# Optimization experiments

Hardware: AMD Instinct MI355X
Metric: run time of the kernel (lower is better)

## Reference

```python
import jax, jax.numpy as jnp
import numpy as np

B, C, W, H = 16, 512, 32, 32


def spatial_shift1(y):
    # y: [B, W, H, C]; quartile-wise shifts with edge rows/cols left unchanged
    c = y.shape[-1]
    cq = c // 4
    p0 = jnp.concatenate([y[:, :1, :, 0*cq:1*cq], y[:, :-1, :, 0*cq:1*cq]], axis=1)  # w <- w-1
    p1 = jnp.concatenate([y[:, 1:, :, 1*cq:2*cq], y[:, -1:, :, 1*cq:2*cq]], axis=1)  # w <- w+1
    p2 = jnp.concatenate([y[:, :, :1, 2*cq:3*cq], y[:, :, :-1, 2*cq:3*cq]], axis=2)  # h <- h-1
    p3 = jnp.concatenate([y[:, :, 1:, 3*cq:], y[:, :, -1:, 3*cq:]], axis=2)          # h <- h+1
    return jnp.concatenate([p0, p1, p2, p3], axis=-1)


def spatial_shift2(y):
    # same as shift1 with w/h roles swapped
    c = y.shape[-1]
    cq = c // 4
    p0 = jnp.concatenate([y[:, :, :1, 0*cq:1*cq], y[:, :, :-1, 0*cq:1*cq]], axis=2)  # h <- h-1
    p1 = jnp.concatenate([y[:, :, 1:, 1*cq:2*cq], y[:, :, -1:, 1*cq:2*cq]], axis=2)  # h <- h+1
    p2 = jnp.concatenate([y[:, :1, :, 2*cq:3*cq], y[:, :-1, :, 2*cq:3*cq]], axis=1)  # w <- w-1
    p3 = jnp.concatenate([y[:, 1:, :, 3*cq:], y[:, -1:, :, 3*cq:]], axis=1)          # w <- w+1
    return jnp.concatenate([p0, p1, p2, p3], axis=-1)


def setup_inputs() -> dict:
    key = jax.random.key(0)
    ks = jax.random.split(key, 9)
    s = 0.02
    return {
        "x": jax.random.normal(ks[0], (B, C, W, H), dtype=jnp.float32),
        "w1": jax.random.normal(ks[1], (3 * C, C), dtype=jnp.float32) * s,
        "b1": jax.random.normal(ks[2], (3 * C,), dtype=jnp.float32) * s,
        "wa": jax.random.normal(ks[3], (C, C), dtype=jnp.float32) * s,
        "ba": jax.random.normal(ks[4], (C,), dtype=jnp.float32) * s,
        "wb": jax.random.normal(ks[5], (3 * C, C), dtype=jnp.float32) * s,
        "bb": jax.random.normal(ks[6], (3 * C,), dtype=jnp.float32) * s,
        "w2": jax.random.normal(ks[7], (C, C), dtype=jnp.float32) * s,
        "b2": jax.random.normal(ks[8], (C,), dtype=jnp.float32) * s,
    }


def reference(x, w1, b1, wa, ba, wb, bb, w2, b2):
    c = x.shape[1]
    xp = jnp.transpose(x, (0, 2, 3, 1))                     # [B, W, H, C]
    y = jnp.einsum("bwhc,oc->bwho", xp, w1) + b1            # [B, W, H, 3C]
    x1 = spatial_shift1(y[..., :c])
    x2 = spatial_shift2(y[..., c:2 * c])
    x3 = y[..., 2 * c:]
    # SplitAttention: descriptor a = sum over branches and spatial positions
    a = jnp.sum(x1 + x2 + x3, axis=(1, 2))                  # [B, C]
    hat = jax.nn.gelu(a @ wa.T + ba, approximate=False) @ wb.T + bb  # [B, 3C]
    bar = jax.nn.softmax(hat.reshape(-1, 3, c), axis=1)     # softmax over k=3
    g = bar[:, :, None, None, :]                            # [B, 3, 1, 1, C]
    out = g[:, 0] * x1 + g[:, 1] * x2 + g[:, 2] * x3        # [B, W, H, C]
    z = jnp.einsum("bwhc,oc->bwho", out, w2) + b2           # [B, W, H, C]
    return jnp.transpose(z, (0, 3, 1, 2))                   # [B, C, W, H]
```

## Files before the change

kernel.cpp:

```cpp
#include <hip/hip_runtime.h>
#include <stdint.h>

typedef __bf16 bf16x8 __attribute__((ext_vector_type(8)));
typedef float f32x4 __attribute__((ext_vector_type(4)));

#define B_ 16
#define C_ 512
#define S_ 1024
#define N1 1536

__device__ inline unsigned short f2b(float f) {
    unsigned int u = __builtin_bit_cast(unsigned int, f);
    unsigned int lsb = (u >> 16) & 1u;
    u += 0x7fffu + lsb;
    return (unsigned short)(u >> 16);
}
__device__ inline float b2f(unsigned int s) {
    unsigned int u = (s & 0xffffu) << 16;
    return __builtin_bit_cast(float, u);
}

__global__ void transpose_convert_x(const float* __restrict__ x, unsigned short* __restrict__ xT) {
    __shared__ float tile[32][33];
    int b = blockIdx.z;
    int c0 = blockIdx.y * 32;
    int s0 = blockIdx.x * 32;
    int tx = threadIdx.x, ty = threadIdx.y;
    const float* xp = x + ((size_t)b * C_ + c0) * S_ + s0;
#pragma unroll
    for (int i = 0; i < 4; i++)
        tile[ty + i * 8][tx] = xp[(size_t)(ty + i * 8) * S_ + tx];
    __syncthreads();
    unsigned short* op = xT + ((size_t)b * S_ + s0) * C_ + c0;
#pragma unroll
    for (int i = 0; i < 4; i++)
        op[(size_t)(ty + i * 8) * C_ + tx] = f2b(tile[tx][ty + i * 8]);
}

__global__ void convert_f32_bf16(const float* __restrict__ src, unsigned short* __restrict__ dst, int n4) {
    int i = blockIdx.x * blockDim.x + threadIdx.x;
    if (i < n4) {
        float4 v = ((const float4*)src)[i];
        ((ushort4*)dst)[i] = make_ushort4(f2b(v.x), f2b(v.y), f2b(v.z), f2b(v.w));
    }
}

__global__ void zero_f32(float* __restrict__ p, int n) {
    int i = blockIdx.x * blockDim.x + threadIdx.x;
    if (i < n) p[i] = 0.0f;
}

template <bool TRANS_OUT>
__global__ __launch_bounds__(256) void gemm_bf16(
    const unsigned short* __restrict__ A,
    const unsigned short* __restrict__ Wt,
    const float* __restrict__ bias,
    void* __restrict__ Cout,
    int N)
{
    const int K = 512;
    __shared__ __align__(16) unsigned short As[128 * 40];
    __shared__ __align__(16) unsigned short Bs[128 * 40];
    int m0 = blockIdx.x * 128;
    int n0 = blockIdx.y * 128;
    int tid = threadIdx.x;
    int lane = tid & 63, wid = tid >> 6;
    int wm = (wid >> 1) * 64, wn = (wid & 1) * 64;
    int quad = lane >> 4, l16 = lane & 15;

    f32x4 acc[4][4] = {};

    for (int kt = 0; kt < K; kt += 32) {
        __syncthreads();
#pragma unroll
        for (int r = 0; r < 2; r++) {
            int ch = tid + r * 256;
            int m = ch >> 2, kc = ch & 3;
            *(uint4*)(&As[m * 40 + kc * 8]) = *(const uint4*)(&A[(size_t)(m0 + m) * K + kt + kc * 8]);
            *(uint4*)(&Bs[m * 40 + kc * 8]) = *(const uint4*)(&Wt[(size_t)(n0 + m) * K + kt + kc * 8]);
        }
        __syncthreads();
        bf16x8 af[4], bf[4];
#pragma unroll
        for (int t = 0; t < 4; t++) {
            af[t] = *(const bf16x8*)(&As[(wm + t * 16 + l16) * 40 + quad * 8]);
            bf[t] = *(const bf16x8*)(&Bs[(wn + t * 16 + l16) * 40 + quad * 8]);
        }
#pragma unroll
        for (int mt = 0; mt < 4; mt++)
#pragma unroll
            for (int nt = 0; nt < 4; nt++)
                acc[mt][nt] = __builtin_amdgcn_mfma_f32_16x16x32_bf16(af[mt], bf[nt], acc[mt][nt], 0, 0, 0);
    }

#pragma unroll
    for (int mt = 0; mt < 4; mt++) {
#pragma unroll
        for (int nt = 0; nt < 4; nt++) {
            int n = n0 + wn + nt * 16 + l16;
            float bv = bias[n];
            int mbase = m0 + wm + mt * 16 + quad * 4;
            if (!TRANS_OUT) {
                unsigned short* Y = (unsigned short*)Cout;
#pragma unroll
                for (int r = 0; r < 4; r++)
                    Y[(size_t)(mbase + r) * N + n] = f2b(acc[mt][nt][r] + bv);
            } else {
                float* Z = (float*)Cout;
                int b = mbase >> 10;
                int s = mbase & 1023;
                float4 v = make_float4(acc[mt][nt][0] + bv, acc[mt][nt][1] + bv,
                                       acc[mt][nt][2] + bv, acc[mt][nt][3] + bv);
                *(float4*)(&Z[((size_t)(b * 512 + n)) * 1024 + s]) = v;
            }
        }
    }
}


__global__ void asum_kernel(const unsigned short* __restrict__ y, float* __restrict__ a) {
    int b = blockIdx.y;
    int w0 = blockIdx.x * 2;
    int t = threadIdx.x;
    int c = t * 2;
    int q = c >> 7;
    int dw1 = (q == 0) ? -1 : (q == 1) ? 1 : 0;
    int dh1 = (q == 2) ? -1 : (q == 3) ? 1 : 0;
    int dh2 = (q == 0) ? -1 : (q == 1) ? 1 : 0;
    int dw2 = (q == 2) ? -1 : (q == 3) ? 1 : 0;
    float s0 = 0.f, s1 = 0.f;
    size_t base = (size_t)b * S_;
    for (int p = 0; p < 64; p++) {
        int w = w0 + (p >> 5);
        int h = p & 31;
        int w1i = min(max(w + dw1, 0), 31), h1i = min(max(h + dh1, 0), 31);
        int w2i = min(max(w + dw2, 0), 31), h2i = min(max(h + dh2, 0), 31);
        unsigned int v1 = *(const unsigned int*)&y[(base + w1i * 32 + h1i) * N1 + c];
        unsigned int v2 = *(const unsigned int*)&y[(base + w2i * 32 + h2i) * N1 + 512 + c];
        unsigned int v3 = *(const unsigned int*)&y[(base + w * 32 + h) * N1 + 1024 + c];
        s0 += b2f(v1) + b2f(v2) + b2f(v3);
        s1 += b2f(v1 >> 16) + b2f(v2 >> 16) + b2f(v3 >> 16);
    }
    atomicAdd(&a[b * 512 + c], s0);
    atomicAdd(&a[b * 512 + c + 1], s1);
}

__global__ __launch_bounds__(256) void mlp_layer1(
    const float* __restrict__ a, const float* __restrict__ wa,
    const float* __restrict__ ba, float* __restrict__ h)
{
    int gw = (blockIdx.x * 256 + threadIdx.x) >> 6;
    int lane = threadIdx.x & 63;
    int b = gw >> 9;
    int o = gw & 511;
    const float4* wr = (const float4*)(wa + (size_t)o * 512);
    const float4* ar = (const float4*)(a + (size_t)b * 512);
    float4 w0 = wr[lane * 2], w1 = wr[lane * 2 + 1];
    float4 a0 = ar[lane * 2], a1 = ar[lane * 2 + 1];
    float dot = w0.x * a0.x + w0.y * a0.y + w0.z * a0.z + w0.w * a0.w
              + w1.x * a1.x + w1.y * a1.y + w1.z * a1.z + w1.w * a1.w;
#pragma unroll
    for (int off = 32; off; off >>= 1) dot += __shfl_down(dot, off);
    if (lane == 0) {
        float v = dot + ba[o];
        h[(size_t)b * 512 + o] = 0.5f * v * (1.0f + erff(v * 0.7071067811865475f));
    }
}

__global__ __launch_bounds__(256) void mlp_layer2(
    const float* __restrict__ h, const float* __restrict__ wb,
    const float* __restrict__ bb, float* __restrict__ hat)
{
    int gw = (blockIdx.x * 256 + threadIdx.x) >> 6;
    int lane = threadIdx.x & 63;
    int b = gw / 1536;
    int o = gw - b * 1536;
    const float4* wr = (const float4*)(wb + (size_t)o * 512);
    const float4* hr = (const float4*)(h + (size_t)b * 512);
    float4 w0 = wr[lane * 2], w1 = wr[lane * 2 + 1];
    float4 h0 = hr[lane * 2], h1 = hr[lane * 2 + 1];
    float dot = w0.x * h0.x + w0.y * h0.y + w0.z * h0.z + w0.w * h0.w
              + w1.x * h1.x + w1.y * h1.y + w1.z * h1.z + w1.w * h1.w;
#pragma unroll
    for (int off = 32; off; off >>= 1) dot += __shfl_down(dot, off);
    if (lane == 0)
        hat[(size_t)b * 1536 + o] = dot + bb[o];
}

__global__ __launch_bounds__(256) void softmax_gate(
    const float* __restrict__ hat, float* __restrict__ g)
{
    int i = blockIdx.x * 256 + threadIdx.x;
    int b = i >> 9, c = i & 511;
    float h0 = hat[(size_t)b * 1536 + c];
    float h1 = hat[(size_t)b * 1536 + 512 + c];
    float h2 = hat[(size_t)b * 1536 + 1024 + c];
    float mx = fmaxf(h0, fmaxf(h1, h2));
    float e0 = __expf(h0 - mx), e1 = __expf(h1 - mx), e2 = __expf(h2 - mx);
    float inv = 1.0f / (e0 + e1 + e2);
    g[(b * 3 + 0) * 512 + c] = e0 * inv;
    g[(b * 3 + 1) * 512 + c] = e1 * inv;
    g[(b * 3 + 2) * 512 + c] = e2 * inv;
}

__global__ void combine_kernel(const unsigned short* __restrict__ y,
                               const float* __restrict__ g,
                               unsigned short* __restrict__ outT)
{
    int b = blockIdx.y;
    int w = blockIdx.x;
    int t = threadIdx.x;
    int c = t * 2;
    int q = c >> 7;
    int dw1 = (q == 0) ? -1 : (q == 1) ? 1 : 0;
    int dh1 = (q == 2) ? -1 : (q == 3) ? 1 : 0;
    int dh2 = (q == 0) ? -1 : (q == 1) ? 1 : 0;
    int dw2 = (q == 2) ? -1 : (q == 3) ? 1 : 0;
    float g00 = g[(b * 3 + 0) * 512 + c], g01 = g[(b * 3 + 0) * 512 + c + 1];
    float g10 = g[(b * 3 + 1) * 512 + c], g11 = g[(b * 3 + 1) * 512 + c + 1];
    float g20 = g[(b * 3 + 2) * 512 + c], g21 = g[(b * 3 + 2) * 512 + c + 1];
    int w1i = min(max(w + dw1, 0), 31);
    int w2i = min(max(w + dw2, 0), 31);
    size_t base = (size_t)b * S_;
    for (int h = 0; h < 32; h++) {
        int h1i = min(max(h + dh1, 0), 31);
        int h2i = min(max(h + dh2, 0), 31);
        unsigned int v1 = *(const unsigned int*)&y[(base + w1i * 32 + h1i) * N1 + c];
        unsigned int v2 = *(const unsigned int*)&y[(base + w2i * 32 + h2i) * N1 + 512 + c];
        unsigned int v3 = *(const unsigned int*)&y[(base + w * 32 + h) * N1 + 1024 + c];
        float o0 = g00 * b2f(v1) + g10 * b2f(v2) + g20 * b2f(v3);
        float o1 = g01 * b2f(v1 >> 16) + g11 * b2f(v2 >> 16) + g21 * b2f(v3 >> 16);
        unsigned int ov = (unsigned int)f2b(o0) | ((unsigned int)f2b(o1) << 16);
        *(unsigned int*)&outT[(base + w * 32 + h) * 512 + c] = ov;
    }
}

extern "C" void kernel_launch(void* const* d_in, const int* in_sizes, int n_in,
                              void* d_out, int out_size, void* d_ws, size_t ws_size,
                              hipStream_t stream) {
    const float* x  = (const float*)d_in[0];
    const float* w1 = (const float*)d_in[1];
    const float* b1 = (const float*)d_in[2];
    const float* wa = (const float*)d_in[3];
    const float* ba = (const float*)d_in[4];
    const float* wb = (const float*)d_in[5];
    const float* bb = (const float*)d_in[6];
    const float* w2 = (const float*)d_in[7];
    const float* b2 = (const float*)d_in[8];
    float* out = (float*)d_out;

    char* ws = (char*)d_ws;
    unsigned short* xT   = (unsigned short*)(ws);
    unsigned short* w1b  = (unsigned short*)(ws + 16777216);
    unsigned short* w2b  = (unsigned short*)(ws + 18350080);
    unsigned short* y    = (unsigned short*)(ws + 18874368);
    float* a_buf         = (float*)(ws + 69206016);
    float* g_buf         = (float*)(ws + 69238784);
    float* h_buf         = (float*)(ws + 69337088);
    float* hat_buf       = (float*)(ws + 69369856);
    unsigned short* outT = (unsigned short*)(ws + 69468160);

    transpose_convert_x<<<dim3(32, 16, 16), dim3(32, 8), 0, stream>>>(x, xT);
    convert_f32_bf16<<<dim3(768), dim3(256), 0, stream>>>(w1, w1b, 196608);
    convert_f32_bf16<<<dim3(256), dim3(256), 0, stream>>>(w2, w2b, 65536);
    gemm_bf16<false><<<dim3(128, 12), dim3(256), 0, stream>>>(xT, w1b, b1, (void*)y, 1536);
    zero_f32<<<dim3(32), dim3(256), 0, stream>>>(a_buf, 8192);
    asum_kernel<<<dim3(16, 16), dim3(256), 0, stream>>>(y, a_buf);
    mlp_layer1<<<dim3(2048), dim3(256), 0, stream>>>(a_buf, wa, ba, h_buf);
    mlp_layer2<<<dim3(6144), dim3(256), 0, stream>>>(h_buf, wb, bb, hat_buf);
    softmax_gate<<<dim3(32), dim3(256), 0, stream>>>(hat_buf, g_buf);
    combine_kernel<<<dim3(32, 16), dim3(256), 0, stream>>>(y, g_buf, outT);
    gemm_bf16<true><<<dim3(128, 4), dim3(256), 0, stream>>>(outT, w2b, b2, (void*)out, 512);
}
```

Before: 217.5 us.

## Fuse shifted-sum descriptor into GEMM epilogue, use direct-to-LDS loads, merge small kernels

```diff
diff --git a/kernel.cpp b/kernel.cpp
--- a/kernel.cpp
+++ b/kernel.cpp
@@ -18,6 +18,13 @@
 __device__ inline float b2f(unsigned int s) {
     unsigned int u = (s & 0xffffu) << 16;
     return __builtin_bit_cast(float, u);
+}
+
+__device__ inline void gl_lds16(const unsigned short* g, unsigned short* l) {
+    __builtin_amdgcn_global_load_lds(
+        (const __attribute__((address_space(1))) void*)(g),
+        (__attribute__((address_space(3))) void*)(l),
+        16, 0, 0);
 }
 
 __global__ void transpose_convert_x(const float* __restrict__ x, unsigned short* __restrict__ xT) {
@@ -37,60 +44,71 @@
         op[(size_t)(ty + i * 8) * C_ + tx] = f2b(tile[tx][ty + i * 8]);
 }
 
-__global__ void convert_f32_bf16(const float* __restrict__ src, unsigned short* __restrict__ dst, int n4) {
-    int i = blockIdx.x * blockDim.x + threadIdx.x;
-    if (i < n4) {
-        float4 v = ((const float4*)src)[i];
-        ((ushort4*)dst)[i] = make_ushort4(f2b(v.x), f2b(v.y), f2b(v.z), f2b(v.w));
-    }
-}
-
-__global__ void zero_f32(float* __restrict__ p, int n) {
-    int i = blockIdx.x * blockDim.x + threadIdx.x;
-    if (i < n) p[i] = 0.0f;
-}
-
-template <bool TRANS_OUT>
+__global__ __launch_bounds__(256) void misc_prep(
+    const float* __restrict__ w1, const float* __restrict__ w2,
+    unsigned short* __restrict__ w1b, unsigned short* __restrict__ w2b,
+    float* __restrict__ sums)
+{
+    int i = blockIdx.x * 256 + threadIdx.x;
+    if (i < 196608) {
+        float4 v = ((const float4*)w1)[i];
+        ((ushort4*)w1b)[i] = make_ushort4(f2b(v.x), f2b(v.y), f2b(v.z), f2b(v.w));
+    } else if (i < 262144) {
+        int j = i - 196608;
+        float4 v = ((const float4*)w2)[j];
+        ((ushort4*)w2b)[j] = make_ushort4(f2b(v.x), f2b(v.y), f2b(v.z), f2b(v.w));
+    } else if (i < 292864) {
+        int j = i - 262144;
+        ((float4*)sums)[j] = make_float4(0.f, 0.f, 0.f, 0.f);
+    }
+}
+
+template <bool TRANS_OUT, bool DO_SUMS>
 __global__ __launch_bounds__(256) void gemm_bf16(
     const unsigned short* __restrict__ A,
     const unsigned short* __restrict__ Wt,
     const float* __restrict__ bias,
-    void* __restrict__ Cout,
-    int N)
+    void* __restrict__ Cout, int N,
+    float* __restrict__ Tsum, float* __restrict__ H0, float* __restrict__ H31,
+    float* __restrict__ C0, float* __restrict__ C31)
 {
     const int K = 512;
-    __shared__ __align__(16) unsigned short As[128 * 40];
-    __shared__ __align__(16) unsigned short Bs[128 * 40];
+    __shared__ __align__(16) unsigned short As[128 * 32];
+    __shared__ __align__(16) unsigned short Bs[128 * 32];
     int m0 = blockIdx.x * 128;
     int n0 = blockIdx.y * 128;
     int tid = threadIdx.x;
     int lane = tid & 63, wid = tid >> 6;
     int wm = (wid >> 1) * 64, wn = (wid & 1) * 64;
     int quad = lane >> 4, l16 = lane & 15;
+    int ch0 = wid * 128 + lane;
+    const unsigned short* Ab = A + (size_t)m0 * K;
+    const unsigned short* Bb = Wt + (size_t)n0 * K;
 
     f32x4 acc[4][4] = {};
 
     for (int kt = 0; kt < K; kt += 32) {
         __syncthreads();
 #pragma unroll
-        for (int r = 0; r < 2; r++) {
-            int ch = tid + r * 256;
+        for (int i = 0; i < 2; i++) {
+            int ch = ch0 + i * 64;
             int m = ch >> 2, kc = ch & 3;
-            *(uint4*)(&As[m * 40 + kc * 8]) = *(const uint4*)(&A[(size_t)(m0 + m) * K + kt + kc * 8]);
-            *(uint4*)(&Bs[m * 40 + kc * 8]) = *(const uint4*)(&Wt[(size_t)(n0 + m) * K + kt + kc * 8]);
+            size_t go = (size_t)m * K + kt + kc * 8;
+            gl_lds16(Ab + go, &As[ch * 8]);
+            gl_lds16(Bb + go, &Bs[ch * 8]);
         }
         __syncthreads();
-        bf16x8 af[4], bf[4];
+        bf16x8 af[4], bfr[4];
 #pragma unroll
         for (int t = 0; t < 4; t++) {
-            af[t] = *(const bf16x8*)(&As[(wm + t * 16 + l16) * 40 + quad * 8]);
-            bf[t] = *(const bf16x8*)(&Bs[(wn + t * 16 + l16) * 40 + quad * 8]);
+            af[t]  = *(const bf16x8*)&As[(wm + t * 16 + l16) * 32 + quad * 8];
+            bfr[t] = *(const bf16x8*)&Bs[(wn + t * 16 + l16) * 32 + quad * 8];
         }
 #pragma unroll
         for (int mt = 0; mt < 4; mt++)
 #pragma unroll
             for (int nt = 0; nt < 4; nt++)
-                acc[mt][nt] = __builtin_amdgcn_mfma_f32_16x16x32_bf16(af[mt], bf[nt], acc[mt][nt], 0, 0, 0);
+                acc[mt][nt] = __builtin_amdgcn_mfma_f32_16x16x32_bf16(af[mt], bfr[nt], acc[mt][nt], 0, 0, 0);
     }
 
 #pragma unroll
@@ -115,55 +133,92 @@
             }
         }
     }
-}
-
-
-__global__ void asum_kernel(const unsigned short* __restrict__ y, float* __restrict__ a) {
-    int b = blockIdx.y;
-    int w0 = blockIdx.x * 2;
+
+    if (DO_SUMS) {
+        int b = m0 >> 10;
+        int wlo = (m0 & 1023) >> 5;
+#pragma unroll
+        for (int nt = 0; nt < 4; nt++) {
+            int n = n0 + wn + nt * 16 + l16;
+            float bv = bias[n];
+            float tT = 0.f;
+#pragma unroll
+            for (int mt = 0; mt < 4; mt++)
+#pragma unroll
+                for (int r = 0; r < 4; r++) tT += acc[mt][nt][r] + bv;
+            tT += __shfl_xor(tT, 16);
+            tT += __shfl_xor(tT, 32);
+            if (quad == 0) {
+                atomicAdd(&Tsum[b * 1536 + n], tT);
+                float th0 = acc[0][nt][0] + acc[2][nt][0] + 2.f * bv;
+                atomicAdd(&H0[b * 1536 + n], th0);
+            }
+            if (quad == 3) {
+                float th31 = acc[1][nt][3] + acc[3][nt][3] + 2.f * bv;
+                atomicAdd(&H31[b * 1536 + n], th31);
+            }
+            if (wlo == 0 && wm == 0) {
+                float tc = 0.f;
+#pragma unroll
+                for (int mt = 0; mt < 2; mt++)
+#pragma unroll
+                    for (int r = 0; r < 4; r++) tc += acc[mt][nt][r] + bv;
+                tc += __shfl_xor(tc, 16);
+                tc += __shfl_xor(tc, 32);
+                if (quad == 0) atomicAdd(&C0[b * 1536 + n], tc);
+            }
+            if (wlo == 28 && wm == 64) {
+                float tc = 0.f;
+#pragma unroll
+                for (int mt = 2; mt < 4; mt++)
+#pragma unroll
+                    for (int r = 0; r < 4; r++) tc += acc[mt][nt][r] + bv;
+                tc += __shfl_xor(tc, 16);
+                tc += __shfl_xor(tc, 32);
+                if (quad == 0) atomicAdd(&C31[b * 1536 + n], tc);
+            }
+        }
+    }
+}
+
+__global__ __launch_bounds__(256) void mlp_layer1(
+    const float* __restrict__ sums, const float* __restrict__ wa,
+    const float* __restrict__ ba, float* __restrict__ h)
+{
+    __shared__ float sa[512];
+    int b = blockIdx.x >> 7;
     int t = threadIdx.x;
-    int c = t * 2;
-    int q = c >> 7;
-    int dw1 = (q == 0) ? -1 : (q == 1) ? 1 : 0;
-    int dh1 = (q == 2) ? -1 : (q == 3) ? 1 : 0;
-    int dh2 = (q == 0) ? -1 : (q == 1) ? 1 : 0;
-    int dw2 = (q == 2) ? -1 : (q == 3) ? 1 : 0;
-    float s0 = 0.f, s1 = 0.f;
-    size_t base = (size_t)b * S_;
-    for (int p = 0; p < 64; p++) {
-        int w = w0 + (p >> 5);
-        int h = p & 31;
-        int w1i = min(max(w + dw1, 0), 31), h1i = min(max(h + dh1, 0), 31);
-        int w2i = min(max(w + dw2, 0), 31), h2i = min(max(h + dh2, 0), 31);
-        unsigned int v1 = *(const unsigned int*)&y[(base + w1i * 32 + h1i) * N1 + c];
-        unsigned int v2 = *(const unsigned int*)&y[(base + w2i * 32 + h2i) * N1 + 512 + c];
-        unsigned int v3 = *(const unsigned int*)&y[(base + w * 32 + h) * N1 + 1024 + c];
-        s0 += b2f(v1) + b2f(v2) + b2f(v3);
-        s1 += b2f(v1 >> 16) + b2f(v2 >> 16) + b2f(v3 >> 16);
-    }
-    atomicAdd(&a[b * 512 + c], s0);
-    atomicAdd(&a[b * 512 + c + 1], s1);
-}
-
-__global__ __launch_bounds__(256) void mlp_layer1(
-    const float* __restrict__ a, const float* __restrict__ wa,
-    const float* __restrict__ ba, float* __restrict__ h)
-{
-    int gw = (blockIdx.x * 256 + threadIdx.x) >> 6;
-    int lane = threadIdx.x & 63;
-    int b = gw >> 9;
-    int o = gw & 511;
+    const float* Tp   = sums;
+    const float* H0p  = sums + 24576;
+    const float* H31p = sums + 49152;
+    const float* C0p  = sums + 73728;
+    const float* C31p = sums + 98304;
+#pragma unroll
+    for (int j = 0; j < 2; j++) {
+        int c = t + j * 256;
+        int q = c >> 7;
+        int n1 = b * 1536 + c;
+        float t123 = Tp[n1] + Tp[n1 + 512] + Tp[n1 + 1024];
+        float sC1 = C0p[n1] - C31p[n1];
+        float sH1 = H0p[n1] - H31p[n1];
+        float sC2 = C0p[n1 + 512] - C31p[n1 + 512];
+        float sH2 = H0p[n1 + 512] - H31p[n1 + 512];
+        float e = (q < 2) ? (sC1 + sH2) : (sH1 + sC2);
+        sa[c] = t123 + ((q & 1) ? -e : e);
+    }
+    __syncthreads();
+    int lane = t & 63, wid = t >> 6;
+    int o = (blockIdx.x & 127) * 4 + wid;
     const float4* wr = (const float4*)(wa + (size_t)o * 512);
-    const float4* ar = (const float4*)(a + (size_t)b * 512);
-    float4 w0 = wr[lane * 2], w1 = wr[lane * 2 + 1];
-    float4 a0 = ar[lane * 2], a1 = ar[lane * 2 + 1];
+    float4 w0 = wr[lane * 2], w1v = wr[lane * 2 + 1];
+    float4 a0 = ((const float4*)sa)[lane * 2], a1 = ((const float4*)sa)[lane * 2 + 1];
     float dot = w0.x * a0.x + w0.y * a0.y + w0.z * a0.z + w0.w * a0.w
-              + w1.x * a1.x + w1.y * a1.y + w1.z * a1.z + w1.w * a1.w;
+              + w1v.x * a1.x + w1v.y * a1.y + w1v.z * a1.z + w1v.w * a1.w;
 #pragma unroll
     for (int off = 32; off; off >>= 1) dot += __shfl_down(dot, off);
     if (lane == 0) {
         float v = dot + ba[o];
-        h[(size_t)b * 512 + o] = 0.5f * v * (1.0f + erff(v * 0.7071067811865475f));
+        h[b * 512 + o] = 0.5f * v * (1.0f + erff(v * 0.7071067811865475f));
     }
 }
 
@@ -187,51 +242,52 @@
         hat[(size_t)b * 1536 + o] = dot + bb[o];
 }
 
-__global__ __launch_bounds__(256) void softmax_gate(
-    const float* __restrict__ hat, float* __restrict__ g)
-{
-    int i = blockIdx.x * 256 + threadIdx.x;
-    int b = i >> 9, c = i & 511;
-    float h0 = hat[(size_t)b * 1536 + c];
-    float h1 = hat[(size_t)b * 1536 + 512 + c];
-    float h2 = hat[(size_t)b * 1536 + 1024 + c];
-    float mx = fmaxf(h0, fmaxf(h1, h2));
-    float e0 = __expf(h0 - mx), e1 = __expf(h1 - mx), e2 = __expf(h2 - mx);
-    float inv = 1.0f / (e0 + e1 + e2);
-    g[(b * 3 + 0) * 512 + c] = e0 * inv;
-    g[(b * 3 + 1) * 512 + c] = e1 * inv;
-    g[(b * 3 + 2) * 512 + c] = e2 * inv;
-}
-
-__global__ void combine_kernel(const unsigned short* __restrict__ y,
-                               const float* __restrict__ g,
-                               unsigned short* __restrict__ outT)
+__global__ __launch_bounds__(256) void combine_softmax(
+    const unsigned short* __restrict__ y, const float* __restrict__ hat,
+    unsigned short* __restrict__ outT)
 {
     int b = blockIdx.y;
-    int w = blockIdx.x;
     int t = threadIdx.x;
-    int c = t * 2;
-    int q = c >> 7;
+    int w = blockIdx.x * 4 + (t >> 6);
+    int c8 = (t & 63) * 8;
+    int q = c8 >> 7;
     int dw1 = (q == 0) ? -1 : (q == 1) ? 1 : 0;
     int dh1 = (q == 2) ? -1 : (q == 3) ? 1 : 0;
     int dh2 = (q == 0) ? -1 : (q == 1) ? 1 : 0;
     int dw2 = (q == 2) ? -1 : (q == 3) ? 1 : 0;
-    float g00 = g[(b * 3 + 0) * 512 + c], g01 = g[(b * 3 + 0) * 512 + c + 1];
-    float g10 = g[(b * 3 + 1) * 512 + c], g11 = g[(b * 3 + 1) * 512 + c + 1];
-    float g20 = g[(b * 3 + 2) * 512 + c], g21 = g[(b * 3 + 2) * 512 + c + 1];
+    float g0[8], g1[8], g2[8];
+#pragma unroll
+    for (int j = 0; j < 8; j++) {
+        int c = c8 + j;
+        float h0 = hat[b * 1536 + c];
+        float h1 = hat[b * 1536 + 512 + c];
+        float h2 = hat[b * 1536 + 1024 + c];
+        float mx = fmaxf(h0, fmaxf(h1, h2));
+        float e0 = __expf(h0 - mx), e1 = __expf(h1 - mx), e2 = __expf(h2 - mx);
+        float inv = 1.0f / (e0 + e1 + e2);
+        g0[j] = e0 * inv; g1[j] = e1 * inv; g2[j] = e2 * inv;
+    }
     int w1i = min(max(w + dw1, 0), 31);
     int w2i = min(max(w + dw2, 0), 31);
     size_t base = (size_t)b * S_;
     for (int h = 0; h < 32; h++) {
         int h1i = min(max(h + dh1, 0), 31);
         int h2i = min(max(h + dh2, 0), 31);
-        unsigned int v1 = *(const unsigned int*)&y[(base + w1i * 32 + h1i) * N1 + c];
-        unsigned int v2 = *(const unsigned int*)&y[(base + w2i * 32 + h2i) * N1 + 512 + c];
-        unsigned int v3 = *(const unsigned int*)&y[(base + w * 32 + h) * N1 + 1024 + c];
-        float o0 = g00 * b2f(v1) + g10 * b2f(v2) + g20 * b2f(v3);
-        float o1 = g01 * b2f(v1 >> 16) + g11 * b2f(v2 >> 16) + g21 * b2f(v3 >> 16);
-        unsigned int ov = (unsigned int)f2b(o0) | ((unsigned int)f2b(o1) << 16);
-        *(unsigned int*)&outT[(base + w * 32 + h) * 512 + c] = ov;
+        uint4 u1 = *(const uint4*)&y[(base + w1i * 32 + h1i) * N1 + c8];
+        uint4 u2 = *(const uint4*)&y[(base + w2i * 32 + h2i) * N1 + 512 + c8];
+        uint4 u3 = *(const uint4*)&y[(base + w * 32 + h) * N1 + 1024 + c8];
+        unsigned int p[4];
+        const unsigned int* a1 = &u1.x;
+        const unsigned int* a2 = &u2.x;
+        const unsigned int* a3 = &u3.x;
+#pragma unroll
+        for (int k = 0; k < 4; k++) {
+            int j = k * 2;
+            float lo = g0[j] * b2f(a1[k]) + g1[j] * b2f(a2[k]) + g2[j] * b2f(a3[k]);
+            float hi = g0[j + 1] * b2f(a1[k] >> 16) + g1[j + 1] * b2f(a2[k] >> 16) + g2[j + 1] * b2f(a3[k] >> 16);
+            p[k] = (unsigned int)f2b(lo) | ((unsigned int)f2b(hi) << 16);
+        }
+        *(uint4*)&outT[(base + w * 32 + h) * 512 + c8] = make_uint4(p[0], p[1], p[2], p[3]);
     }
 }
 
@@ -251,24 +307,27 @@
 
     char* ws = (char*)d_ws;
     unsigned short* xT   = (unsigned short*)(ws);
+    unsigned short* outT = (unsigned short*)(ws);
     unsigned short* w1b  = (unsigned short*)(ws + 16777216);
     unsigned short* w2b  = (unsigned short*)(ws + 18350080);
     unsigned short* y    = (unsigned short*)(ws + 18874368);
-    float* a_buf         = (float*)(ws + 69206016);
-    float* g_buf         = (float*)(ws + 69238784);
-    float* h_buf         = (float*)(ws + 69337088);
-    float* hat_buf       = (float*)(ws + 69369856);
-    unsigned short* outT = (unsigned short*)(ws + 69468160);
+    float* sums          = (float*)(ws + 69206016);
+    float* h_buf         = (float*)(ws + 69697536);
+    float* hat_buf       = (float*)(ws + 69730304);
+
+    float* Tsum = sums;
+    float* H0   = sums + 24576;
+    float* H31  = sums + 49152;
+    float* C0   = sums + 73728;
+    float* C31  = sums + 98304;
 
     transpose_convert_x<<<dim3(32, 16, 16), dim3(32, 8), 0, stream>>>(x, xT);
-    convert_f32_bf16<<<dim3(768), dim3(256), 0, stream>>>(w1, w1b, 196608);
-    convert_f32_bf16<<<dim3(256), dim3(256), 0, stream>>>(w2, w2b, 65536);
-    gemm_bf16<false><<<dim3(128, 12), dim3(256), 0, stream>>>(xT, w1b, b1, (void*)y, 1536);
-    zero_f32<<<dim3(32), dim3(256), 0, stream>>>(a_buf, 8192);
-    asum_kernel<<<dim3(16, 16), dim3(256), 0, stream>>>(y, a_buf);
-    mlp_layer1<<<dim3(2048), dim3(256), 0, stream>>>(a_buf, wa, ba, h_buf);
+    misc_prep<<<dim3(1144), dim3(256), 0, stream>>>(w1, w2, w1b, w2b, sums);
+    gemm_bf16<false, true><<<dim3(128, 12), dim3(256), 0, stream>>>(
+        xT, w1b, b1, (void*)y, 1536, Tsum, H0, H31, C0, C31);
+    mlp_layer1<<<dim3(2048), dim3(256), 0, stream>>>(sums, wa, ba, h_buf);
     mlp_layer2<<<dim3(6144), dim3(256), 0, stream>>>(h_buf, wb, bb, hat_buf);
-    softmax_gate<<<dim3(32), dim3(256), 0, stream>>>(hat_buf, g_buf);
-    combine_kernel<<<dim3(32, 16), dim3(256), 0, stream>>>(y, g_buf, outT);
-    gemm_bf16<true><<<dim3(128, 4), dim3(256), 0, stream>>>(outT, w2b, b2, (void*)out, 512);
-}
+    combine_softmax<<<dim3(8, 16), dim3(256), 0, stream>>>(y, hat_buf, outT);
+    gemm_bf16<true, false><<<dim3(128, 4), dim3(256), 0, stream>>>(
+        outT, w2b, b2, (void*)out, 512, nullptr, nullptr, nullptr, nullptr, nullptr);
+}
```

New measurement: 193.4 us. -11.1%, faster.
